# Performance work log

Hardware: AMD Instinct MI355X
Metric: run time of the kernel (lower is better)

The kernel has to match this reference:

```python
import jax, jax.numpy as jnp
import numpy as np

NUM_EXPERTS = 8
TOP_K = 2
HIDDEN = 2048
INTER = 768


def setup_inputs() -> dict:
    key = jax.random.key(0)
    k0, k1, k2, k3, k4 = jax.random.split(key, 5)
    return {
        "hidden_states": jax.random.normal(k0, (2, 1024, HIDDEN), jnp.float32),
        "gate_w": jax.random.normal(k1, (NUM_EXPERTS, HIDDEN), jnp.float32) * 0.02,
        "w_gate": jax.random.normal(k2, (NUM_EXPERTS, HIDDEN, INTER), jnp.float32) * 0.02,
        "w_up": jax.random.normal(k3, (NUM_EXPERTS, HIDDEN, INTER), jnp.float32) * 0.02,
        "w_down": jax.random.normal(k4, (NUM_EXPERTS, INTER, HIDDEN), jnp.float32) * 0.02,
    }


def reference(hidden_states, gate_w, w_gate, w_up, w_down):
    B, S, H = hidden_states.shape
    x = hidden_states.reshape(-1, H)            # [T, H]
    T = x.shape[0]

    # Router: softmax in fp32, top-k, renormalize (norm_topk_prob=True)
    router_logits = jnp.einsum('td,ed->te', x, gate_w)          # [T, E]
    probs = jax.nn.softmax(router_logits.astype(jnp.float32), axis=-1)
    top_w, top_i = jax.lax.top_k(probs, TOP_K)                  # [T, K]
    top_w = top_w / jnp.sum(top_w, axis=-1, keepdims=True)
    top_w = top_w.astype(x.dtype)

    # Dense combine weights [T, E]: zero for unselected experts.
    # (top-k indices are distinct per token, so .set is exact.)
    w_dense = jnp.zeros((T, NUM_EXPERTS), x.dtype).at[
        jnp.arange(T)[:, None], top_i].set(top_w)

    # Per-expert SwiGLU MLP (Qwen3MoeMLP): down(silu(gate(x)) * up(x)).
    # EP dispatch/combine with ep_size=1 is an identity permutation, so the
    # math equals running every selected (token, expert) pair and combining.
    g = jax.nn.silu(jnp.einsum('td,edf->etf', x, w_gate))       # [E, T, F]
    u = jnp.einsum('td,edf->etf', x, w_up)                      # [E, T, F]
    y = jnp.einsum('etf,efd->etd', g * u, w_down)               # [E, T, H]

    out = jnp.einsum('etd,te->td', y, w_dense)                  # [T, H]
    return out.reshape(B, S, H), router_logits
```

## Files before the change

### kernel.cpp

```cpp
#include <hip/hip_runtime.h>
#include <hip/hip_bf16.h>
#include <math.h>

#define NTOK 2048
#define HID 2048
#define NEXP 8
#define FINT 768
#define TOPK 2

typedef __attribute__((ext_vector_type(8))) short bf16x8;
typedef __attribute__((ext_vector_type(4))) float f32x4;

static __device__ __forceinline__ unsigned short f2bf(float f) {
    union { float f; unsigned u; } v; v.f = f;
    unsigned r = v.u + 0x7fffu + ((v.u >> 16) & 1u);
    return (unsigned short)(r >> 16);
}

static __device__ __forceinline__ void gl16(const void* g, void* l) {
    __builtin_amdgcn_global_load_lds(
        (const __attribute__((address_space(1))) unsigned int*)g,
        (__attribute__((address_space(3))) unsigned int*)(uintptr_t)l,
        16, 0, 0);
}


__global__ __launch_bounds__(256) void moe_router_cvt(
        const float* __restrict__ x,
        const float* __restrict__ gw,
        float* __restrict__ logits_out,
        int* __restrict__ topk_idx,
        float* __restrict__ topk_w,
        unsigned short* __restrict__ xb) {
    int w = threadIdx.x >> 6, l = threadIdx.x & 63;
    int t = blockIdx.x * 4 + w;
    const float4* xr = (const float4*)(x + (size_t)t * HID);
    unsigned short* xbr = xb + (size_t)t * HID;
    float4 v[8];
    #pragma unroll
    for (int i = 0; i < 8; ++i) v[i] = xr[i * 64 + l];
    #pragma unroll
    for (int i = 0; i < 8; ++i)
        *(ushort4*)&xbr[(i * 64 + l) * 4] =
            make_ushort4(f2bf(v[i].x), f2bf(v[i].y), f2bf(v[i].z), f2bf(v[i].w));
    float acc[NEXP];
    #pragma unroll
    for (int e = 0; e < NEXP; ++e) {
        const float4* gr = (const float4*)(gw + (size_t)e * HID);
        float a = 0.f;
        #pragma unroll
        for (int i = 0; i < 8; ++i) {
            float4 g = gr[i * 64 + l];
            a += v[i].x * g.x + v[i].y * g.y + v[i].z * g.z + v[i].w * g.w;
        }
        acc[e] = a;
    }
    #pragma unroll
    for (int off = 32; off > 0; off >>= 1)
        #pragma unroll
        for (int e = 0; e < NEXP; ++e) acc[e] += __shfl_xor(acc[e], off);
    if (l == 0) {
        float m = -1e30f;
        #pragma unroll
        for (int i = 0; i < NEXP; ++i) m = fmaxf(m, acc[i]);
        float p[NEXP];
        #pragma unroll
        for (int i = 0; i < NEXP; ++i) p[i] = expf(acc[i] - m);
        int i0 = 0;
        #pragma unroll
        for (int i = 1; i < NEXP; ++i) if (p[i] > p[i0]) i0 = i;
        int i1 = (i0 == 0) ? 1 : 0;
        #pragma unroll
        for (int i = 0; i < NEXP; ++i) if (i != i0 && p[i] > p[i1]) i1 = i;
        float w0 = p[i0], w1 = p[i1], sw = w0 + w1;
        topk_idx[t * 2 + 0] = i0;
        topk_idx[t * 2 + 1] = i1;
        topk_w[t * 2 + 0] = w0 / sw;
        topk_w[t * 2 + 1] = w1 / sw;
        #pragma unroll
        for (int i = 0; i < NEXP; ++i) logits_out[(size_t)t * NEXP + i] = acc[i];
    }
}

__global__ void moe_build_kernel(const int* __restrict__ topk_idx,
                                 const float* __restrict__ topk_w,
                                 int* __restrict__ counts,
                                 int* __restrict__ offsets,
                                 int* __restrict__ elist_t,
                                 float* __restrict__ elist_w,
                                 int* __restrict__ row_token,
                                 float* __restrict__ row_w) {
    __shared__ int scnt[NEXP];
    __shared__ int soff[NEXP];
    int tid = threadIdx.x;
    if (tid < NEXP) scnt[tid] = 0;
    __syncthreads();
    for (int t = tid; t < NTOK; t += 1024) {
        #pragma unroll
        for (int k = 0; k < TOPK; ++k) {
            int e = topk_idx[t * 2 + k];
            float w = topk_w[t * 2 + k];
            int slot = atomicAdd(&scnt[e], 1);
            elist_t[e * NTOK + slot] = t;
            elist_w[e * NTOK + slot] = w;
        }
    }
    __syncthreads();
    if (tid == 0) {
        int o = 0;
        for (int e = 0; e < NEXP; ++e) {
            soff[e] = o; offsets[e] = o; counts[e] = scnt[e]; o += scnt[e];
        }
    }
    __syncthreads();
    for (int e = 0; e < NEXP; ++e) {
        int c = scnt[e], o = soff[e];
        for (int s = tid; s < c; s += 1024) {
            row_token[o + s] = elist_t[e * NTOK + s];
            row_w[o + s]     = elist_w[e * NTOK + s];
        }
    }
}

__global__ __launch_bounds__(256) void transpose_cvt_all(
        const float* __restrict__ wg, const float* __restrict__ wu,
        const float* __restrict__ wd,
        unsigned short* __restrict__ wgt, unsigned short* __restrict__ wut,
        unsigned short* __restrict__ wdt) {
    int e = blockIdx.y;
    int idx = blockIdx.x;
    const float* src; unsigned short* dst; int R, C, tr, tc;
    if (idx < 384)      { src = wg; dst = wgt; R = HID;  C = FINT; tr = idx / 12; tc = idx % 12; }
    else if (idx < 768) { idx -= 384; src = wu; dst = wut; R = HID;  C = FINT; tr = idx / 12; tc = idx % 12; }
    else                { idx -= 768; src = wd; dst = wdt; R = FINT; C = HID;  tr = idx / 32; tc = idx % 32; }
    int r0 = tr * 64, c0 = tc * 64;
    src += (size_t)e * R * C;
    dst += (size_t)e * R * C;
    __shared__ __align__(16) float tile[64 * 64];
    int tid = threadIdx.x;
    {
        int rbase = tid >> 4;
        int ch = tid & 15;
        #pragma unroll
        for (int i = 0; i < 4; ++i) {
            int row = i * 16 + rbase;
            float4 v = *(const float4*)&src[(size_t)(r0 + row) * C + c0 + ch * 4];
            int p = ch ^ (row & 15);
            *(float4*)&tile[row * 64 + p * 4] = v;
        }
    }
    __syncthreads();
    {
        int r16 = (tid & 15) * 4;
        int cg = tid >> 4;
        float4 v[4];
        #pragma unroll
        for (int j = 0; j < 4; ++j) {
            int row = r16 + j;
            int p = cg ^ (row & 15);
            v[j] = *(const float4*)&tile[row * 64 + p * 4];
        }
        #pragma unroll
        for (int i = 0; i < 4; ++i) {
            float c0v, c1v, c2v, c3v;
            c0v = (i == 0) ? v[0].x : (i == 1) ? v[0].y : (i == 2) ? v[0].z : v[0].w;
            c1v = (i == 0) ? v[1].x : (i == 1) ? v[1].y : (i == 2) ? v[1].z : v[1].w;
            c2v = (i == 0) ? v[2].x : (i == 1) ? v[2].y : (i == 2) ? v[2].z : v[2].w;
            c3v = (i == 0) ? v[3].x : (i == 1) ? v[3].y : (i == 2) ? v[3].z : v[3].w;
            ushort4 o = make_ushort4(f2bf(c0v), f2bf(c1v), f2bf(c2v), f2bf(c3v));
            *(uint2*)&dst[(size_t)(c0 + cg * 4 + i) * R + r0 + r16] = *(const uint2*)&o;
        }
    }
}

__global__ __launch_bounds__(256) void moe_stage_a_mfma(
        const unsigned short* __restrict__ xb,
        const unsigned short* __restrict__ wgt,
        const unsigned short* __restrict__ wut,
        const int* __restrict__ counts,
        const int* __restrict__ offsets,
        const int* __restrict__ row_token,
        unsigned short* __restrict__ h_buf) {
    int e = blockIdx.x, mt = blockIdx.y, nt = blockIdx.z;
    int count = counts[e];
    int m0 = mt * 64;
    if (m0 >= count) return;
    int off = offsets[e];
    int n0 = nt * 64;
    int mcnt = min(64, count - m0);
    int tid = threadIdx.x;

    __shared__ __align__(16) unsigned short As[2][64 * 64];
    __shared__ __align__(16) unsigned short Bg[2][64 * 64];
    __shared__ __align__(16) unsigned short Bu[2][64 * 64];
    __shared__ int toks[64];
    if (tid < 64) toks[tid] = row_token[off + m0 + min(tid, mcnt - 1)];
    __syncthreads();

    int w = tid >> 6, l = tid & 63;
    int wr = w >> 1, wc = w & 1;
    int lr = l & 15, lh = l >> 4;
    int rA = w * 8 + (l >> 3);
    int cA = l & 7;

    const unsigned short* wgE = wgt + (size_t)e * FINT * HID + (size_t)n0 * HID;
    const unsigned short* wuE = wut + (size_t)e * FINT * HID + (size_t)n0 * HID;

    f32x4 gacc[2][2] = {};
    f32x4 uacc[2][2] = {};

    auto STAGE = [&](int buf, int k0) {
        #pragma unroll
        for (int i = 0; i < 2; ++i) {
            int row = 32 * i + rA;
            int sc = (cA ^ (row & 7)) << 3;
            size_t db = (size_t)(32 * i + w * 8) * 128;
            gl16(xb + (size_t)toks[row] * HID + k0 + sc, (char*)&As[buf][0] + db);
            gl16(wgE + (size_t)row * HID + k0 + sc,      (char*)&Bg[buf][0] + db);
            gl16(wuE + (size_t)row * HID + k0 + sc,      (char*)&Bu[buf][0] + db);
        }
    };

    auto COMPUTE = [&](int buf) {
        #pragma unroll
        for (int ks = 0; ks < 2; ++ks) {
            bf16x8 af[2], bg[2], bu[2];
            #pragma unroll
            for (int mi = 0; mi < 2; ++mi) {
                int row = wr * 32 + mi * 16 + lr;
                int byte = row * 128 + ((ks * 64 + lh * 16) ^ ((row & 7) << 4));
                af[mi] = *(const bf16x8*)((const char*)&As[buf][0] + byte);
            }
            #pragma unroll
            for (int ni = 0; ni < 2; ++ni) {
                int row = wc * 32 + ni * 16 + lr;
                int byte = row * 128 + ((ks * 64 + lh * 16) ^ ((row & 7) << 4));
                bg[ni] = *(const bf16x8*)((const char*)&Bg[buf][0] + byte);
                bu[ni] = *(const bf16x8*)((const char*)&Bu[buf][0] + byte);
            }
            #pragma unroll
            for (int mi = 0; mi < 2; ++mi)
                #pragma unroll
                for (int ni = 0; ni < 2; ++ni) {
                    gacc[mi][ni] = __builtin_amdgcn_mfma_f32_16x16x32_bf16(af[mi], bg[ni], gacc[mi][ni], 0, 0, 0);
                    uacc[mi][ni] = __builtin_amdgcn_mfma_f32_16x16x32_bf16(af[mi], bu[ni], uacc[mi][ni], 0, 0, 0);
                }
        }
    };

    STAGE(0, 0);
    __syncthreads();
    for (int t = 0; t < HID / 64; ++t) {
        int cur = t & 1;
        if (t + 1 < HID / 64) STAGE(cur ^ 1, (t + 1) * 64);
        COMPUTE(cur);
        __syncthreads();
    }

    #pragma unroll
    for (int mi = 0; mi < 2; ++mi)
        #pragma unroll
        for (int ni = 0; ni < 2; ++ni)
            #pragma unroll
            for (int j = 0; j < 4; ++j) {
                int row = wr * 32 + mi * 16 + lh * 4 + j;
                if (row < mcnt) {
                    int col = wc * 32 + ni * 16 + lr;
                    float g = gacc[mi][ni][j], u = uacc[mi][ni][j];
                    float hv = g / (1.f + expf(-g)) * u;
                    h_buf[(size_t)(off + m0 + row) * FINT + n0 + col] = f2bf(hv);
                }
            }
}

__global__ __launch_bounds__(256) void moe_stage_b_mfma(
        const unsigned short* __restrict__ h_buf,
        const unsigned short* __restrict__ wdt,
        const int* __restrict__ counts,
        const int* __restrict__ offsets,
        const int* __restrict__ row_token,
        const float* __restrict__ row_w,
        float* __restrict__ out) {
    int e = blockIdx.x, mt = blockIdx.y, nt = blockIdx.z;
    int count = counts[e];
    int m0 = mt * 128;
    if (m0 >= count) return;
    int off = offsets[e];
    int n0 = nt * 128;
    int mcnt = min(128, count - m0);
    int tid = threadIdx.x;

    __shared__ __align__(16) unsigned short As[2][128 * 64];
    __shared__ __align__(16) unsigned short Bs[2][128 * 64];
    __shared__ int toks[128];
    __shared__ float rws[128];
    if (tid < 128) {
        int mm = min(tid, mcnt - 1);
        toks[tid] = row_token[off + m0 + mm];
        rws[tid] = row_w[off + m0 + mm];
    }
    __syncthreads();

    int w = tid >> 6, l = tid & 63;
    int wr = w >> 1, wc = w & 1;
    int lr = l & 15, lh = l >> 4;
    int wbase = (tid & 192) * 16;

    const unsigned short* hb = h_buf + (size_t)(off + m0) * FINT;
    const unsigned short* wdE = wdt + (size_t)e * HID * FINT + (size_t)n0 * FINT;

    f32x4 acc[4][4] = {};

    auto STAGE = [&](int buf, int k0) {
        #pragma unroll
        for (int i = 0; i < 4; ++i) {
            int s = i * 256 + tid;
            int row = s >> 3, c = s & 7;
            int sc = (c ^ (row & 7)) << 3;
            gl16(hb + (size_t)row * FINT + k0 + sc,  (char*)&As[buf][0] + i * 4096 + wbase);
            gl16(wdE + (size_t)row * FINT + k0 + sc, (char*)&Bs[buf][0] + i * 4096 + wbase);
        }
    };

    auto COMPUTE = [&](int buf) {
        #pragma unroll
        for (int ks = 0; ks < 2; ++ks) {
            bf16x8 af[4], bf[4];
            #pragma unroll
            for (int mi = 0; mi < 4; ++mi) {
                int row = wr * 64 + mi * 16 + lr;
                int byte = row * 128 + ((ks * 64 + lh * 16) ^ ((row & 7) << 4));
                af[mi] = *(const bf16x8*)((const char*)&As[buf][0] + byte);
            }
            #pragma unroll
            for (int ni = 0; ni < 4; ++ni) {
                int row = wc * 64 + ni * 16 + lr;
                int byte = row * 128 + ((ks * 64 + lh * 16) ^ ((row & 7) << 4));
                bf[ni] = *(const bf16x8*)((const char*)&Bs[buf][0] + byte);
            }
            #pragma unroll
            for (int mi = 0; mi < 4; ++mi)
                #pragma unroll
                for (int ni = 0; ni < 4; ++ni)
                    acc[mi][ni] = __builtin_amdgcn_mfma_f32_16x16x32_bf16(af[mi], bf[ni], acc[mi][ni], 0, 0, 0);
        }
    };

    STAGE(0, 0);
    __syncthreads();
    for (int t = 0; t < FINT / 64; ++t) {
        int cur = t & 1;
        if (t + 1 < FINT / 64) STAGE(cur ^ 1, (t + 1) * 64);
        COMPUTE(cur);
        __syncthreads();
    }

    #pragma unroll
    for (int mi = 0; mi < 4; ++mi)
        #pragma unroll
        for (int ni = 0; ni < 4; ++ni)
            #pragma unroll
            for (int j = 0; j < 4; ++j) {
                int row = wr * 64 + mi * 16 + lh * 4 + j;
                if (row < mcnt) {
                    int col = n0 + wc * 64 + ni * 16 + lr;
                    atomicAdd(&out[(size_t)toks[row] * HID + col],
                              rws[row] * acc[mi][ni][j]);
                }
            }
}

extern "C" void kernel_launch(void* const* d_in, const int* in_sizes, int n_in,
                              void* d_out, int out_size, void* d_ws, size_t ws_size,
                              hipStream_t stream) {
    const float* x       = (const float*)d_in[0];
    const float* gate_w  = (const float*)d_in[1];
    const float* w_gate  = (const float*)d_in[2];
    const float* w_up    = (const float*)d_in[3];
    const float* w_down  = (const float*)d_in[4];
    float* out = (float*)d_out;

    char* ws = (char*)d_ws;
    int*   topk_idx  = (int*)  (ws + 0);
    float* topk_w    = (float*)(ws + 16384);
    int*   counts    = (int*)  (ws + 32768);
    int*   offsets   = (int*)  (ws + 32800);
    int*   row_token = (int*)  (ws + 33024);
    float* row_w     = (float*)(ws + 49408);
    int*   elist_t   = (int*)  (ws + 65792);
    float* elist_w   = (float*)(ws + 131328);

    unsigned short* xb   = (unsigned short*)(ws + 196864);
    unsigned short* wg_t = (unsigned short*)(ws + 8585472);
    unsigned short* wu_t = (unsigned short*)(ws + 33751296);
    unsigned short* wd_t = (unsigned short*)(ws + 58917120);
    unsigned short* hb   = (unsigned short*)(ws + 84082944);

    float* logits_out = out + (size_t)NTOK * HID;

    hipMemsetAsync(out, 0, (size_t)NTOK * HID * sizeof(float), stream);

    moe_router_cvt<<<NTOK / 4, 256, 0, stream>>>(x, gate_w, logits_out,
                                                 topk_idx, topk_w, xb);
    moe_build_kernel<<<1, 1024, 0, stream>>>(topk_idx, topk_w, counts, offsets,
                                             elist_t, elist_w, row_token, row_w);
    dim3 gT(1152, NEXP);
    transpose_cvt_all<<<gT, 256, 0, stream>>>(w_gate, w_up, w_down,
                                              wg_t, wu_t, wd_t);

    dim3 gridA(NEXP, NTOK / 64, FINT / 64);
    moe_stage_a_mfma<<<gridA, 256, 0, stream>>>(xb, wg_t, wu_t, counts, offsets,
                                                row_token, hb);
    dim3 gridB(NEXP, NTOK / 128, HID / 128);
    moe_stage_b_mfma<<<gridB, 256, 0, stream>>>(hb, wd_t, counts, offsets,
                                                row_token, row_w, out);
}
```

Measured before the change: 161.0 us.

## Fuse weight transposes into router and stage-A kernels as extra blocks

The standalone weight transpose/convert kernel is split up: the gate/up weight transposes become extra blocks of the router kernel, and the down-projection transpose becomes extra blocks of the stage-A GEMM kernel. This removes a kernel launch and its serialization point, and lets independent work overlap within one grid. Stage-A's shared memory is now one raw buffer sized for both roles, and its grid is flattened with experts interleaved. The down-weight transpose blocks now share a grid with GEMM blocks that use more shared memory, which may affect occupancy.

```diff
diff --git a/kernel.cpp b/kernel.cpp
--- a/kernel.cpp
+++ b/kernel.cpp
@@ -25,60 +25,113 @@
 }
 
 
-__global__ __launch_bounds__(256) void moe_router_cvt(
+static __device__ __forceinline__ void transpose_tile(
+        const float* __restrict__ src, unsigned short* __restrict__ dst,
+        int R, int C, int r0, int c0, float* tile, int tid) {
+    {
+        int rbase = tid >> 4;
+        int ch = tid & 15;
+        #pragma unroll
+        for (int i = 0; i < 4; ++i) {
+            int row = i * 16 + rbase;
+            float4 v = *(const float4*)&src[(size_t)(r0 + row) * C + c0 + ch * 4];
+            int p = ch ^ (row & 15);
+            *(float4*)&tile[row * 64 + p * 4] = v;
+        }
+    }
+    __syncthreads();
+    {
+        int r16 = (tid & 15) * 4;
+        int cg = tid >> 4;
+        float4 v[4];
+        #pragma unroll
+        for (int j = 0; j < 4; ++j) {
+            int row = r16 + j;
+            int p = cg ^ (row & 15);
+            v[j] = *(const float4*)&tile[row * 64 + p * 4];
+        }
+        #pragma unroll
+        for (int i = 0; i < 4; ++i) {
+            float c0v = (i == 0) ? v[0].x : (i == 1) ? v[0].y : (i == 2) ? v[0].z : v[0].w;
+            float c1v = (i == 0) ? v[1].x : (i == 1) ? v[1].y : (i == 2) ? v[1].z : v[1].w;
+            float c2v = (i == 0) ? v[2].x : (i == 1) ? v[2].y : (i == 2) ? v[2].z : v[2].w;
+            float c3v = (i == 0) ? v[3].x : (i == 1) ? v[3].y : (i == 2) ? v[3].z : v[3].w;
+            ushort4 o = make_ushort4(f2bf(c0v), f2bf(c1v), f2bf(c2v), f2bf(c3v));
+            *(uint2*)&dst[(size_t)(c0 + cg * 4 + i) * R + r0 + r16] = *(const uint2*)&o;
+        }
+    }
+}
+
+__global__ __launch_bounds__(256) void k1_router_wgwu(
         const float* __restrict__ x,
         const float* __restrict__ gw,
+        const float* __restrict__ wg, const float* __restrict__ wu,
         float* __restrict__ logits_out,
         int* __restrict__ topk_idx,
         float* __restrict__ topk_w,
-        unsigned short* __restrict__ xb) {
-    int w = threadIdx.x >> 6, l = threadIdx.x & 63;
-    int t = blockIdx.x * 4 + w;
-    const float4* xr = (const float4*)(x + (size_t)t * HID);
-    unsigned short* xbr = xb + (size_t)t * HID;
-    float4 v[8];
-    #pragma unroll
-    for (int i = 0; i < 8; ++i) v[i] = xr[i * 64 + l];
-    #pragma unroll
-    for (int i = 0; i < 8; ++i)
-        *(ushort4*)&xbr[(i * 64 + l) * 4] =
-            make_ushort4(f2bf(v[i].x), f2bf(v[i].y), f2bf(v[i].z), f2bf(v[i].w));
-    float acc[NEXP];
-    #pragma unroll
-    for (int e = 0; e < NEXP; ++e) {
-        const float4* gr = (const float4*)(gw + (size_t)e * HID);
-        float a = 0.f;
-        #pragma unroll
-        for (int i = 0; i < 8; ++i) {
-            float4 g = gr[i * 64 + l];
-            a += v[i].x * g.x + v[i].y * g.y + v[i].z * g.z + v[i].w * g.w;
-        }
-        acc[e] = a;
-    }
-    #pragma unroll
-    for (int off = 32; off > 0; off >>= 1)
-        #pragma unroll
-        for (int e = 0; e < NEXP; ++e) acc[e] += __shfl_xor(acc[e], off);
-    if (l == 0) {
-        float m = -1e30f;
-        #pragma unroll
-        for (int i = 0; i < NEXP; ++i) m = fmaxf(m, acc[i]);
-        float p[NEXP];
-        #pragma unroll
-        for (int i = 0; i < NEXP; ++i) p[i] = expf(acc[i] - m);
-        int i0 = 0;
-        #pragma unroll
-        for (int i = 1; i < NEXP; ++i) if (p[i] > p[i0]) i0 = i;
-        int i1 = (i0 == 0) ? 1 : 0;
-        #pragma unroll
-        for (int i = 0; i < NEXP; ++i) if (i != i0 && p[i] > p[i1]) i1 = i;
-        float w0 = p[i0], w1 = p[i1], sw = w0 + w1;
-        topk_idx[t * 2 + 0] = i0;
-        topk_idx[t * 2 + 1] = i1;
-        topk_w[t * 2 + 0] = w0 / sw;
-        topk_w[t * 2 + 1] = w1 / sw;
-        #pragma unroll
-        for (int i = 0; i < NEXP; ++i) logits_out[(size_t)t * NEXP + i] = acc[i];
+        unsigned short* __restrict__ xb,
+        unsigned short* __restrict__ wgt, unsigned short* __restrict__ wut) {
+    __shared__ __align__(16) float tile[64 * 64];
+    int bid = blockIdx.x;
+    if (bid < 512) {
+        int w = threadIdx.x >> 6, l = threadIdx.x & 63;
+        int t = bid * 4 + w;
+        const float4* xr = (const float4*)(x + (size_t)t * HID);
+        unsigned short* xbr = xb + (size_t)t * HID;
+        float4 v[8];
+        #pragma unroll
+        for (int i = 0; i < 8; ++i) v[i] = xr[i * 64 + l];
+        #pragma unroll
+        for (int i = 0; i < 8; ++i)
+            *(ushort4*)&xbr[(i * 64 + l) * 4] =
+                make_ushort4(f2bf(v[i].x), f2bf(v[i].y), f2bf(v[i].z), f2bf(v[i].w));
+        float acc[NEXP];
+        #pragma unroll
+        for (int e = 0; e < NEXP; ++e) {
+            const float4* gr = (const float4*)(gw + (size_t)e * HID);
+            float a = 0.f;
+            #pragma unroll
+            for (int i = 0; i < 8; ++i) {
+                float4 g = gr[i * 64 + l];
+                a += v[i].x * g.x + v[i].y * g.y + v[i].z * g.z + v[i].w * g.w;
+            }
+            acc[e] = a;
+        }
+        #pragma unroll
+        for (int off = 32; off > 0; off >>= 1)
+            #pragma unroll
+            for (int e = 0; e < NEXP; ++e) acc[e] += __shfl_xor(acc[e], off);
+        if (l == 0) {
+            float m = -1e30f;
+            #pragma unroll
+            for (int i = 0; i < NEXP; ++i) m = fmaxf(m, acc[i]);
+            float p[NEXP];
+            #pragma unroll
+            for (int i = 0; i < NEXP; ++i) p[i] = expf(acc[i] - m);
+            int i0 = 0;
+            #pragma unroll
+            for (int i = 1; i < NEXP; ++i) if (p[i] > p[i0]) i0 = i;
+            int i1 = (i0 == 0) ? 1 : 0;
+            #pragma unroll
+            for (int i = 0; i < NEXP; ++i) if (i != i0 && p[i] > p[i1]) i1 = i;
+            float w0 = p[i0], w1 = p[i1], sw = w0 + w1;
+            topk_idx[t * 2 + 0] = i0;
+            topk_idx[t * 2 + 1] = i1;
+            topk_w[t * 2 + 0] = w0 / sw;
+            topk_w[t * 2 + 1] = w1 / sw;
+            #pragma unroll
+            for (int i = 0; i < NEXP; ++i) logits_out[(size_t)t * NEXP + i] = acc[i];
+        }
+    } else {
+        int idx = bid - 512;
+        int e = idx / 768, sub = idx % 768;
+        const float* src; unsigned short* dst;
+        if (sub < 384) { src = wg; dst = wgt; }
+        else           { src = wu; dst = wut; sub -= 384; }
+        int tr = sub / 12, tc = sub % 12;
+        src += (size_t)e * HID * FINT;
+        dst += (size_t)e * HID * FINT;
+        transpose_tile(src, dst, HID, FINT, tr * 64, tc * 64, tile, threadIdx.x);
     }
 }
 
@@ -122,78 +175,41 @@
     }
 }
 
-__global__ __launch_bounds__(256) void transpose_cvt_all(
-        const float* __restrict__ wg, const float* __restrict__ wu,
-        const float* __restrict__ wd,
-        unsigned short* __restrict__ wgt, unsigned short* __restrict__ wut,
-        unsigned short* __restrict__ wdt) {
-    int e = blockIdx.y;
-    int idx = blockIdx.x;
-    const float* src; unsigned short* dst; int R, C, tr, tc;
-    if (idx < 384)      { src = wg; dst = wgt; R = HID;  C = FINT; tr = idx / 12; tc = idx % 12; }
-    else if (idx < 768) { idx -= 384; src = wu; dst = wut; R = HID;  C = FINT; tr = idx / 12; tc = idx % 12; }
-    else                { idx -= 768; src = wd; dst = wdt; R = FINT; C = HID;  tr = idx / 32; tc = idx % 32; }
-    int r0 = tr * 64, c0 = tc * 64;
-    src += (size_t)e * R * C;
-    dst += (size_t)e * R * C;
-    __shared__ __align__(16) float tile[64 * 64];
-    int tid = threadIdx.x;
-    {
-        int rbase = tid >> 4;
-        int ch = tid & 15;
-        #pragma unroll
-        for (int i = 0; i < 4; ++i) {
-            int row = i * 16 + rbase;
-            float4 v = *(const float4*)&src[(size_t)(r0 + row) * C + c0 + ch * 4];
-            int p = ch ^ (row & 15);
-            *(float4*)&tile[row * 64 + p * 4] = v;
-        }
-    }
-    __syncthreads();
-    {
-        int r16 = (tid & 15) * 4;
-        int cg = tid >> 4;
-        float4 v[4];
-        #pragma unroll
-        for (int j = 0; j < 4; ++j) {
-            int row = r16 + j;
-            int p = cg ^ (row & 15);
-            v[j] = *(const float4*)&tile[row * 64 + p * 4];
-        }
-        #pragma unroll
-        for (int i = 0; i < 4; ++i) {
-            float c0v, c1v, c2v, c3v;
-            c0v = (i == 0) ? v[0].x : (i == 1) ? v[0].y : (i == 2) ? v[0].z : v[0].w;
-            c1v = (i == 0) ? v[1].x : (i == 1) ? v[1].y : (i == 2) ? v[1].z : v[1].w;
-            c2v = (i == 0) ? v[2].x : (i == 1) ? v[2].y : (i == 2) ? v[2].z : v[2].w;
-            c3v = (i == 0) ? v[3].x : (i == 1) ? v[3].y : (i == 2) ? v[3].z : v[3].w;
-            ushort4 o = make_ushort4(f2bf(c0v), f2bf(c1v), f2bf(c2v), f2bf(c3v));
-            *(uint2*)&dst[(size_t)(c0 + cg * 4 + i) * R + r0 + r16] = *(const uint2*)&o;
-        }
-    }
-}
-
-__global__ __launch_bounds__(256) void moe_stage_a_mfma(
+__global__ __launch_bounds__(256) void k3_stagea_wd(
         const unsigned short* __restrict__ xb,
         const unsigned short* __restrict__ wgt,
         const unsigned short* __restrict__ wut,
+        const float* __restrict__ wd,
+        unsigned short* __restrict__ wdt,
         const int* __restrict__ counts,
         const int* __restrict__ offsets,
         const int* __restrict__ row_token,
         unsigned short* __restrict__ h_buf) {
-    int e = blockIdx.x, mt = blockIdx.y, nt = blockIdx.z;
+    __shared__ __align__(16) char smem[49408];
+    int bid = blockIdx.x;
+    int tid = threadIdx.x;
+
+    if (bid < 3072) {
+        int e = bid / 384, sub = bid % 384;
+        int tr = sub / 32, tc = sub % 32;
+        transpose_tile(wd + (size_t)e * FINT * HID,
+                       wdt + (size_t)e * FINT * HID,
+                       FINT, HID, tr * 64, tc * 64, (float*)smem, tid);
+        return;
+    }
+    int b = bid - 3072;
+    int e = b & 7, mt = (b >> 3) & 31, nt = b >> 8;
     int count = counts[e];
     int m0 = mt * 64;
     if (m0 >= count) return;
     int off = offsets[e];
     int n0 = nt * 64;
     int mcnt = min(64, count - m0);
-    int tid = threadIdx.x;
-
-    __shared__ __align__(16) unsigned short As[2][64 * 64];
-    __shared__ __align__(16) unsigned short Bg[2][64 * 64];
-    __shared__ __align__(16) unsigned short Bu[2][64 * 64];
-    __shared__ int toks[64];
+
+    char* AsB = smem;
+    char* BgB = smem + 16384;
+    char* BuB = smem + 32768;
+    int* toks = (int*)(smem + 49152);
     if (tid < 64) toks[tid] = row_token[off + m0 + min(tid, mcnt - 1)];
     __syncthreads();
 
@@ -214,10 +230,10 @@
         for (int i = 0; i < 2; ++i) {
             int row = 32 * i + rA;
             int sc = (cA ^ (row & 7)) << 3;
-            size_t db = (size_t)(32 * i + w * 8) * 128;
-            gl16(xb + (size_t)toks[row] * HID + k0 + sc, (char*)&As[buf][0] + db);
-            gl16(wgE + (size_t)row * HID + k0 + sc,      (char*)&Bg[buf][0] + db);
-            gl16(wuE + (size_t)row * HID + k0 + sc,      (char*)&Bu[buf][0] + db);
+            size_t db = (size_t)buf * 8192 + (size_t)(32 * i + w * 8) * 128;
+            gl16(xb + (size_t)toks[row] * HID + k0 + sc, AsB + db);
+            gl16(wgE + (size_t)row * HID + k0 + sc,      BgB + db);
+            gl16(wuE + (size_t)row * HID + k0 + sc,      BuB + db);
         }
     };
 
@@ -228,15 +244,15 @@
             #pragma unroll
             for (int mi = 0; mi < 2; ++mi) {
                 int row = wr * 32 + mi * 16 + lr;
-                int byte = row * 128 + ((ks * 64 + lh * 16) ^ ((row & 7) << 4));
-                af[mi] = *(const bf16x8*)((const char*)&As[buf][0] + byte);
+                int byte = buf * 8192 + row * 128 + ((ks * 64 + lh * 16) ^ ((row & 7) << 4));
+                af[mi] = *(const bf16x8*)(AsB + byte);
             }
             #pragma unroll
             for (int ni = 0; ni < 2; ++ni) {
                 int row = wc * 32 + ni * 16 + lr;
-                int byte = row * 128 + ((ks * 64 + lh * 16) ^ ((row & 7) << 4));
-                bg[ni] = *(const bf16x8*)((const char*)&Bg[buf][0] + byte);
-                bu[ni] = *(const bf16x8*)((const char*)&Bu[buf][0] + byte);
+                int byte = buf * 8192 + row * 128 + ((ks * 64 + lh * 16) ^ ((row & 7) << 4));
+                bg[ni] = *(const bf16x8*)(BgB + byte);
+                bu[ni] = *(const bf16x8*)(BuB + byte);
             }
             #pragma unroll
             for (int mi = 0; mi < 2; ++mi)
@@ -400,17 +416,12 @@
 
     hipMemsetAsync(out, 0, (size_t)NTOK * HID * sizeof(float), stream);
 
-    moe_router_cvt<<<NTOK / 4, 256, 0, stream>>>(x, gate_w, logits_out,
-                                                 topk_idx, topk_w, xb);
+    k1_router_wgwu<<<512 + 6144, 256, 0, stream>>>(
+        x, gate_w, w_gate, w_up, logits_out, topk_idx, topk_w, xb, wg_t, wu_t);
     moe_build_kernel<<<1, 1024, 0, stream>>>(topk_idx, topk_w, counts, offsets,
                                              elist_t, elist_w, row_token, row_w);
-    dim3 gT(1152, NEXP);
-    transpose_cvt_all<<<gT, 256, 0, stream>>>(w_gate, w_up, w_down,
-                                              wg_t, wu_t, wd_t);
-
-    dim3 gridA(NEXP, NTOK / 64, FINT / 64);
-    moe_stage_a_mfma<<<gridA, 256, 0, stream>>>(xb, wg_t, wu_t, counts, offsets,
-                                                row_token, hb);
+    k3_stagea_wd<<<3072 + 3072, 256, 0, stream>>>(
+        xb, wg_t, wu_t, w_down, wd_t, counts, offsets, row_token, hb);
     dim3 gridB(NEXP, NTOK / 128, HID / 128);
     moe_stage_b_mfma<<<gridB, 256, 0, stream>>>(hb, wd_t, counts, offsets,
                                                 row_token, row_w, out);
```

After: 152.4 us. -5.3%, faster.
